# Optimization experiments

Measured on AMD Instinct MI355X. Metric: run time of the kernel, lower is better.

The kernel has to match this reference:

```python
import jax, jax.numpy as jnp
import numpy as np

B, T, C = 2, 2048, 2048
H, HD = 16, 128  # num_heads, head_dim; inner_dim = H*HD = C
EPS = 1e-8


def _hadamard(n):
    # Sylvester construction, orthonormal scaling 1/sqrt(n)
    h = np.array([[1.0]], dtype=np.float32)
    while h.shape[0] < n:
        h = np.block([[h, h], [h, -h]])
    return jnp.asarray(h / np.sqrt(n), dtype=jnp.float32)


def _round_ste(x):
    # straight-through rounding (matches int8 training-time quantization semantics)
    return x + jax.lax.stop_gradient(jnp.round(x) - x)


def q8_linear(x, w):
    # dynamic per-token int8 activation quant + per-out-channel int8 weight quant
    s_x = jnp.max(jnp.abs(x), axis=-1, keepdims=True) / 127.0 + EPS   # (B,T,1)
    xq = _round_ste(jnp.clip(x / s_x, -127.0, 127.0))
    s_w = jnp.max(jnp.abs(w), axis=-1, keepdims=True) / 127.0 + EPS   # (O,1)
    wq = _round_ste(jnp.clip(w / s_w, -127.0, 127.0))
    return jnp.einsum('btk,ok->bto', xq, wq) * s_x * s_w[:, 0]


def rmsnorm(x, g, eps=1e-6):
    return x * jax.lax.rsqrt(jnp.mean(x * x, axis=-1, keepdims=True) + eps) * g


def apply_rope(x, cos, sin):
    # x: (B,T,H*HD); cos/sin: (T,HD/2); interleaved rotary per head
    b, t, c = x.shape
    xh = x.reshape(b, t, -1, HD)
    x1, x2 = xh[..., 0::2], xh[..., 1::2]
    co = cos[None, :, None, :]
    si = sin[None, :, None, :]
    o1 = x1 * co - x2 * si
    o2 = x1 * si + x2 * co
    out = jnp.stack([o1, o2], axis=-1).reshape(b, t, -1, HD)
    return out.reshape(b, t, c)


def setup_inputs() -> dict:
    key = jax.random.key(0)
    ks = jax.random.split(key, 8)
    hidden_states = jax.random.normal(ks[0], (B, T, C), jnp.float32)
    attention_mask = jax.random.randint(ks[1], (B,), 1, T + 1).astype(jnp.int32)  # valid lengths
    sc = 1.0 / np.sqrt(C)
    wq = jax.random.normal(ks[2], (H * HD, C), jnp.float32) * sc
    wk = jax.random.normal(ks[3], (H * HD, C), jnp.float32) * sc
    wv = jax.random.normal(ks[4], (H * HD, C), jnp.float32) * sc
    wo = jax.random.normal(ks[5], (C, H * HD), jnp.float32) * (1.0 / np.sqrt(H * HD))
    q_gamma = jnp.ones((H * HD,), jnp.float32)
    k_gamma = jnp.ones((H * HD,), jnp.float32)
    inv_freq = 1.0 / (10000.0 ** (np.arange(0, HD, 2, dtype=np.float32) / HD))
    freqs = np.outer(np.arange(T, dtype=np.float32), inv_freq)  # (T, HD/2)
    cos = jnp.asarray(np.cos(freqs), jnp.float32)
    sin = jnp.asarray(np.sin(freqs), jnp.float32)
    return {"hidden_states": hidden_states, "attention_mask": attention_mask,
            "wq": wq, "wk": wk, "wv": wv, "wo": wo,
            "q_gamma": q_gamma, "k_gamma": k_gamma, "cos": cos, "sin": sin}


def reference(hidden_states, attention_mask, wq, wk, wv, wo, q_gamma, k_gamma, cos, sin):
    b, t, c = hidden_states.shape
    q = rmsnorm(q8_linear(hidden_states, wq), q_gamma)
    k = rmsnorm(q8_linear(hidden_states, wk), k_gamma)
    v = q8_linear(hidden_states, wv)
    q = apply_rope(q, cos, sin)
    k = apply_rope(k, cos, sin)
    # (B,T,H*HD) -> (B,H,T,HD)
    q = q.reshape(b, t, H, HD).transpose(0, 2, 1, 3)
    k = k.reshape(b, t, H, HD).transpose(0, 2, 1, 3)
    v = v.reshape(b, t, H, HD).transpose(0, 2, 1, 3)
    # Hadamard rotation of q/k head dims (orthonormal -> preserves qk dot products)
    Hm = _hadamard(HD)
    qh = q @ Hm
    kh = k @ Hm
    scores = jnp.einsum('bhqd,bhkd->bhqk', qh, kh) * (1.0 / np.sqrt(HD))
    # ragged batch mask: keys beyond per-batch valid length are masked out
    valid = jnp.arange(t)[None, :] < attention_mask[:, None]   # (B,T)
    scores = jnp.where(valid[:, None, None, :], scores, -1e9)
    p = jax.nn.softmax(scores, axis=-1)
    o = jnp.einsum('bhqk,bhkd->bhqd', p, v)
    o = o.transpose(0, 2, 1, 3).reshape(b, t, c)
    return q8_linear(o, wo)
```

## Files before the change

kernel.cpp:

```cpp
#include <hip/hip_runtime.h>
#include <stdint.h>

typedef unsigned short u16;
typedef unsigned int u32;
typedef int v4i __attribute__((ext_vector_type(4)));
typedef float v4f __attribute__((ext_vector_type(4)));
typedef short v8s __attribute__((ext_vector_type(8)));

#define Bn 2
#define Tn 2048
#define Cn 2048
#define Hn 16
#define HDn 128

__device__ __forceinline__ float b2f(u16 u) {
    u32 x = ((u32)u) << 16;
    float f;
    __builtin_memcpy(&f, &x, 4);
    return f;
}
__device__ __forceinline__ u16 f2b(float f) {
    u32 x;
    __builtin_memcpy(&x, &f, 4);
    u32 r = (x + 0x7fffu + ((x >> 16) & 1u)) >> 16;
    return (u16)r;
}

__device__ __forceinline__ void async16(const void* g, void* l) {
    __builtin_amdgcn_global_load_lds(
        (const __attribute__((address_space(1))) u32*)g,
        (__attribute__((address_space(3))) u32*)l, 16, 0, 0);
}

__global__ __launch_bounds__(256) void quant_all(
    const float* __restrict__ w0, const float* __restrict__ w1,
    const float* __restrict__ w2, const float* __restrict__ w3,
    const float* __restrict__ hid, int8_t* __restrict__ Q,
    float* __restrict__ S) {
    int r = blockIdx.x;
    const float* src;
    int ro;
    if (r < 2048) { src = w0; ro = r; }
    else if (r < 4096) { src = w1; ro = r - 2048; }
    else if (r < 6144) { src = w2; ro = r - 4096; }
    else if (r < 8192) { src = w3; ro = r - 6144; }
    else { src = hid; ro = r - 8192; }
    const float* x = src + (size_t)ro * Cn;
    int tid = threadIdx.x;
    float4 v0 = ((const float4*)x)[tid * 2];
    float4 v1 = ((const float4*)x)[tid * 2 + 1];
    float a[8] = {v0.x, v0.y, v0.z, v0.w, v1.x, v1.y, v1.z, v1.w};
    float m = 0.f;
#pragma unroll
    for (int i = 0; i < 8; i++) m = fmaxf(m, fabsf(a[i]));
#pragma unroll
    for (int o = 32; o; o >>= 1) m = fmaxf(m, __shfl_xor(m, o));
    __shared__ float sm[4];
    if ((tid & 63) == 0) sm[tid >> 6] = m;
    __syncthreads();
    m = fmaxf(fmaxf(sm[0], sm[1]), fmaxf(sm[2], sm[3]));
    float s = m * (1.0f / 127.0f) + 1e-8f;
    if (tid == 0) S[r] = s;
    u32 lo = 0, hi = 0;
#pragma unroll
    for (int i = 0; i < 8; i++) {
        float q = rintf(fminf(127.f, fmaxf(-127.f, a[i] / s)));
        int qi = (int)q;
        u32 byte = (u32)(qi & 0xff);
        if (i < 4) lo |= byte << (8 * i);
        else hi |= byte << (8 * (i - 4));
    }
    u32* qp = (u32*)(Q + (size_t)r * Cn);
    qp[tid * 2] = lo;
    qp[tid * 2 + 1] = hi;
}

__global__ __launch_bounds__(256) void quant_rows(const float* __restrict__ X,
                                                  int8_t* __restrict__ Q,
                                                  float* __restrict__ S) {
    int r = blockIdx.x;
    const float* x = X + (size_t)r * Cn;
    int tid = threadIdx.x;
    float4 v0 = ((const float4*)x)[tid * 2];
    float4 v1 = ((const float4*)x)[tid * 2 + 1];
    float a[8] = {v0.x, v0.y, v0.z, v0.w, v1.x, v1.y, v1.z, v1.w};
    float m = 0.f;
#pragma unroll
    for (int i = 0; i < 8; i++) m = fmaxf(m, fabsf(a[i]));
#pragma unroll
    for (int o = 32; o; o >>= 1) m = fmaxf(m, __shfl_xor(m, o));
    __shared__ float sm[4];
    if ((tid & 63) == 0) sm[tid >> 6] = m;
    __syncthreads();
    m = fmaxf(fmaxf(sm[0], sm[1]), fmaxf(sm[2], sm[3]));
    float s = m * (1.0f / 127.0f) + 1e-8f;
    if (tid == 0) S[r] = s;
    u32 lo = 0, hi = 0;
#pragma unroll
    for (int i = 0; i < 8; i++) {
        float q = rintf(fminf(127.f, fmaxf(-127.f, a[i] / s)));
        int qi = (int)q;
        u32 byte = (u32)(qi & 0xff);
        if (i < 4) lo |= byte << (8 * i);
        else hi |= byte << (8 * (i - 4));
    }
    u32* qp = (u32*)(Q + (size_t)r * Cn);
    qp[tid * 2] = lo;
    qp[tid * 2 + 1] = hi;
}

__global__ __launch_bounds__(256) void gemm_i8(
    const int8_t* __restrict__ A, const int8_t* __restrict__ Bw,
    const float* __restrict__ sA, const float* __restrict__ sB,
    void* __restrict__ Co, long long bStride, long long sbStride,
    long long cStride, int fp32out) {
    int z = blockIdx.z;
    Bw += (size_t)z * bStride;
    sB += (size_t)z * sbStride;
    const int K = 2048, N = 2048;
    __shared__ int8_t As[128 * 64];
    __shared__ int8_t Bs[128 * 64];
    int m0 = blockIdx.x * 128, n0 = blockIdx.y * 128;
    int tid = threadIdx.x, w = tid >> 6, lane = tid & 63;
    int quad = lane >> 4, l15 = lane & 15;
    int wy = w >> 1, wx = w & 1;
    const v4i zi = {0, 0, 0, 0};
    v4i acc[4][4];
#pragma unroll
    for (int i = 0; i < 4; i++)
#pragma unroll
        for (int j = 0; j < 4; j++) acc[i][j] = zi;
    int lrow = lane >> 2;
    int slot = lane & 3;
    int srow = w * 32 + lrow;
    int klog = ((slot ^ (lrow & 3)) * 16);
    const int8_t* ga = A + (size_t)(m0 + srow) * K + klog;
    const int8_t* gb = Bw + (size_t)(n0 + srow) * K + klog;
    int8_t* la = &As[srow * 64 + slot * 16];
    int8_t* lb = &Bs[srow * 64 + slot * 16];
    for (int k0 = 0; k0 < K; k0 += 64) {
        async16(ga + k0, la);
        async16(ga + k0 + (size_t)16 * K, la + 16 * 64);
        async16(gb + k0, lb);
        async16(gb + k0 + (size_t)16 * K, lb + 16 * 64);
        __syncthreads();
        int swz = (quad ^ (l15 & 3)) * 16;
        v4i af[4], bf4[4];
#pragma unroll
        for (int i = 0; i < 4; i++)
            af[i] = *(const v4i*)&As[(wy * 64 + i * 16 + l15) * 64 + swz];
#pragma unroll
        for (int j = 0; j < 4; j++)
            bf4[j] = *(const v4i*)&Bs[(wx * 64 + j * 16 + l15) * 64 + swz];
#pragma unroll
        for (int i = 0; i < 4; i++)
#pragma unroll
            for (int j = 0; j < 4; j++)
                acc[i][j] = __builtin_amdgcn_mfma_i32_16x16x64_i8(
                    af[i], bf4[j], acc[i][j], 0, 0, 0);
        __syncthreads();
    }
#pragma unroll
    for (int i = 0; i < 4; i++) {
        int mb = m0 + wy * 64 + i * 16 + quad * 4;
        float s0 = sA[mb], s1 = sA[mb + 1], s2 = sA[mb + 2], s3 = sA[mb + 3];
#pragma unroll
        for (int j = 0; j < 4; j++) {
            int n = n0 + wx * 64 + j * 16 + l15;
            float sb = sB[n];
            if (fp32out) {
                float* cp = (float*)Co + (size_t)cStride * z + (size_t)mb * N + n;
                cp[0] = (float)acc[i][j][0] * s0 * sb;
                cp[N] = (float)acc[i][j][1] * s1 * sb;
                cp[2 * N] = (float)acc[i][j][2] * s2 * sb;
                cp[3 * N] = (float)acc[i][j][3] * s3 * sb;
            } else {
                u16* cp = (u16*)Co + (size_t)cStride * z + (size_t)mb * N + n;
                cp[0] = f2b((float)acc[i][j][0] * s0 * sb);
                cp[N] = f2b((float)acc[i][j][1] * s1 * sb);
                cp[2 * N] = f2b((float)acc[i][j][2] * s2 * sb);
                cp[3 * N] = f2b((float)acc[i][j][3] * s3 * sb);
            }
        }
    }
}

__global__ __launch_bounds__(256) void norm_rope2(u16* __restrict__ Qb,
                                                  u16* __restrict__ Kb,
                                                  const float* __restrict__ qg,
                                                  const float* __restrict__ kg,
                                                  const float* __restrict__ cs,
                                                  const float* __restrict__ sn) {
    int row = blockIdx.x;
    int isq = row < 4096;
    row &= 4095;
    u16* x = (isq ? Qb : Kb) + (size_t)row * Cn;
    const float* g = isq ? qg : kg;
    float ps = isq ? 0.08838834764831845f : 1.0f;
    int t = row & (Tn - 1);
    int tid = threadIdx.x;
    uint4 raw = ((const uint4*)x)[tid];
    u16 us[8];
    us[0] = raw.x & 0xffff; us[1] = raw.x >> 16;
    us[2] = raw.y & 0xffff; us[3] = raw.y >> 16;
    us[4] = raw.z & 0xffff; us[5] = raw.z >> 16;
    us[6] = raw.w & 0xffff; us[7] = raw.w >> 16;
    float v[8];
#pragma unroll
    for (int i = 0; i < 8; i++) v[i] = b2f(us[i]);
    float ss = 0.f;
#pragma unroll
    for (int i = 0; i < 8; i++) ss += v[i] * v[i];
#pragma unroll
    for (int o = 32; o; o >>= 1) ss += __shfl_xor(ss, o);
    __shared__ float sm[4];
    if ((tid & 63) == 0) sm[tid >> 6] = ss;
    __syncthreads();
    ss = sm[0] + sm[1] + sm[2] + sm[3];
    float r = rsqrtf(ss * (1.f / 2048.f) + 1e-6f) * ps;
    float4 g0 = ((const float4*)g)[tid * 2];
    float4 g1 = ((const float4*)g)[tid * 2 + 1];
    float n[8];
    n[0] = v[0] * r * g0.x; n[1] = v[1] * r * g0.y;
    n[2] = v[2] * r * g0.z; n[3] = v[3] * r * g0.w;
    n[4] = v[4] * r * g1.x; n[5] = v[5] * r * g1.y;
    n[6] = v[6] * r * g1.z; n[7] = v[7] * r * g1.w;
    int pi = (tid & 15) * 4;
    float4 c4 = *(const float4*)(cs + t * 64 + pi);
    float4 s4 = *(const float4*)(sn + t * 64 + pi);
    float o[8];
    o[0] = n[0] * c4.x - n[1] * s4.x; o[1] = n[0] * s4.x + n[1] * c4.x;
    o[2] = n[2] * c4.y - n[3] * s4.y; o[3] = n[2] * s4.y + n[3] * c4.y;
    o[4] = n[4] * c4.z - n[5] * s4.z; o[5] = n[4] * s4.z + n[5] * c4.z;
    o[6] = n[6] * c4.w - n[7] * s4.w; o[7] = n[6] * s4.w + n[7] * c4.w;
    uint4 out;
    out.x = (u32)f2b(o[0]) | ((u32)f2b(o[1]) << 16);
    out.y = (u32)f2b(o[2]) | ((u32)f2b(o[3]) << 16);
    out.z = (u32)f2b(o[4]) | ((u32)f2b(o[5]) << 16);
    out.w = (u32)f2b(o[6]) | ((u32)f2b(o[7]) << 16);
    ((uint4*)x)[tid] = out;
}

__global__ __launch_bounds__(256) void vtrans(const u16* __restrict__ V,
                                              u16* __restrict__ Vt) {
    int bh = blockIdx.y;
    int b = bh >> 4, h = bh & 15;
    int t0 = blockIdx.x * 64;
    __shared__ u32 tile[64][133];
    int tid = threadIdx.x;
    int r = tid >> 2, seg = (tid & 3) * 32;
    const uint4* src =
        (const uint4*)(V + ((size_t)b * Tn + t0 + r) * Cn + h * HDn + seg);
#pragma unroll
    for (int i = 0; i < 4; i++) {
        uint4 u = src[i];
        u32 uu[4] = {u.x, u.y, u.z, u.w};
#pragma unroll
        for (int j = 0; j < 4; j++) {
            tile[r][seg + i * 8 + j * 2] = uu[j] & 0xffff;
            tile[r][seg + i * 8 + j * 2 + 1] = uu[j] >> 16;
        }
    }
    __syncthreads();
    int d = tid >> 1, tseg = (tid & 1) * 32;
    u16* dst = Vt + ((size_t)bh * HDn + d) * Tn + t0 + tseg;
#pragma unroll
    for (int i = 0; i < 4; i++) {
        u32 p0 = tile[tseg + i * 8 + 0][d] | (tile[tseg + i * 8 + 1][d] << 16);
        u32 p1 = tile[tseg + i * 8 + 2][d] | (tile[tseg + i * 8 + 3][d] << 16);
        u32 p2 = tile[tseg + i * 8 + 4][d] | (tile[tseg + i * 8 + 5][d] << 16);
        u32 p3 = tile[tseg + i * 8 + 6][d] | (tile[tseg + i * 8 + 7][d] << 16);
        ((uint4*)dst)[i] = make_uint4(p0, p1, p2, p3);
    }
}

__global__ __launch_bounds__(256, 3) void flash(const u16* __restrict__ Qb,
                                                const u16* __restrict__ Kb,
                                                const u16* __restrict__ Vt,
                                                const int* __restrict__ mask,
                                                float* __restrict__ O) {
    int qt = blockIdx.x, bh = blockIdx.y;
    int b = bh >> 4, h = bh & 15;
    int L = mask[b];
    int nkfull = L >> 6;
    int nk = (L + 63) >> 6;
    __shared__ u16 Ks[64 * 128];
    __shared__ u16 Vs[128 * 64];
    __shared__ u16 Ps[64 * 72];
    __shared__ float sred[256];
    __shared__ float sinv[64];
    int tid = threadIdx.x, w = tid >> 6, lane = tid & 63;
    int quad = lane >> 4, l15 = lane & 15;

    v8s aq[4][4];
#pragma unroll
    for (int i = 0; i < 4; i++)
#pragma unroll
        for (int kk = 0; kk < 4; kk++)
            aq[i][kk] = *(const v8s*)(Qb +
                                      ((size_t)b * Tn + qt * 64 + i * 16 + l15) * Cn +
                                      h * HDn + kk * 32 + quad * 8);

    const u16* ksp[4];
    u16* kdp[4];
    const u16* vsp[4];
    u16* vdp[4];
#pragma unroll
    for (int cc = 0; cc < 4; cc++) {
        int c = w * 4 + cc;
        int rk = c * 4 + (lane >> 4);
        int sk = lane & 15;
        int lgk = sk ^ (rk & 7);
        ksp[cc] = Kb + ((size_t)b * Tn + rk) * Cn + h * HDn + lgk * 8;
        kdp[cc] = Ks + rk * 128 + sk * 8;
        int rv = c * 8 + (lane >> 3);
        int sv = lane & 7;
        int lgv = sv ^ (rv & 7);
        vsp[cc] = Vt + ((size_t)bh * HDn + rv) * Tn + lgv * 8;
        vdp[cc] = Vs + rv * 64 + sv * 8;
    }

    float sum16[16];
#pragma unroll
    for (int j = 0; j < 16; j++) sum16[j] = 0.f;
    const v4f zf = {0.f, 0.f, 0.f, 0.f};
    v4f oacc[4][2];
#pragma unroll
    for (int m = 0; m < 4; m++) {
        oacc[m][0] = zf;
        oacc[m][1] = zf;
    }
    int swz = ((l15 & 7) ^ quad) << 3;

    for (int kt = 0; kt < nk; kt++) {
        __syncthreads();
#pragma unroll
        for (int cc = 0; cc < 4; cc++) async16(ksp[cc], kdp[cc]);
#pragma unroll
        for (int cc = 0; cc < 4; cc++) async16(vsp[cc], vdp[cc]);
#pragma unroll
        for (int cc = 0; cc < 4; cc++) {
            ksp[cc] += 64 * Cn;
            vsp[cc] += 64;
        }
        __syncthreads();
        v4f sacc[4] = {zf, zf, zf, zf};
        const u16* krow = Ks + (w * 16 + l15) * 128;
#pragma unroll
        for (int kk = 0; kk < 4; kk++) {
            v8s bk = *(const v8s*)(krow + ((((kk * 4 + quad) ^ (l15 & 7))) << 3));
#pragma unroll
            for (int i = 0; i < 4; i++)
                sacc[i] = __builtin_amdgcn_mfma_f32_16x16x32_bf16(aq[i][kk], bk,
                                                                  sacc[i], 0, 0, 0);
        }
        bool valid = (kt < nkfull) || ((kt * 64 + w * 16 + l15) < L);
#pragma unroll
        for (int i = 0; i < 4; i++)
#pragma unroll
            for (int r2 = 0; r2 < 4; r2++) {
                float p = valid ? __expf(sacc[i][r2]) : 0.f;
                sum16[i * 4 + r2] += p;
                Ps[(i * 16 + quad * 4 + r2) * 72 + w * 16 + l15] = f2b(p);
            }
        __syncthreads();
#pragma unroll
        for (int kk2 = 0; kk2 < 2; kk2++) {
            v8s ap[4];
#pragma unroll
            for (int m = 0; m < 4; m++)
                ap[m] = *(const v8s*)(Ps + (m * 16 + l15) * 72 + kk2 * 32 + quad * 8);
#pragma unroll
            for (int nbi = 0; nbi < 2; nbi++) {
                int vr = (2 * w + nbi) * 16 + l15;
                v8s bv = *(const v8s*)(Vs + vr * 64 +
                                       ((((kk2 * 4 + quad) ^ (l15 & 7))) << 3));
#pragma unroll
                for (int m = 0; m < 4; m++)
                    oacc[m][nbi] = __builtin_amdgcn_mfma_f32_16x16x32_bf16(
                        ap[m], bv, oacc[m][nbi], 0, 0, 0);
            }
        }
    }
#pragma unroll
    for (int j = 0; j < 16; j++) {
        float s = sum16[j];
        s += __shfl_xor(s, 1);
        s += __shfl_xor(s, 2);
        s += __shfl_xor(s, 4);
        s += __shfl_xor(s, 8);
        sum16[j] = s;
    }
    if (l15 == 0) {
#pragma unroll
        for (int i = 0; i < 4; i++)
#pragma unroll
            for (int r2 = 0; r2 < 4; r2++)
                sred[w * 64 + i * 16 + quad * 4 + r2] = sum16[i * 4 + r2];
    }
    __syncthreads();
    if (tid < 64)
        sinv[tid] =
            1.f / (sred[tid] + sred[64 + tid] + sred[128 + tid] + sred[192 + tid]);
    __syncthreads();
#pragma unroll
    for (int m = 0; m < 4; m++)
#pragma unroll
        for (int r2 = 0; r2 < 4; r2++) {
            float inv = sinv[m * 16 + quad * 4 + r2];
            int row = qt * 64 + m * 16 + quad * 4 + r2;
#pragma unroll
            for (int nbi = 0; nbi < 2; nbi++) {
                int d = h * HDn + (2 * w + nbi) * 16 + l15;
                O[((size_t)b * Tn + row) * Cn + d] = oacc[m][nbi][r2] * inv;
            }
        }
    (void)swz;
}

extern "C" void kernel_launch(void* const* d_in, const int* in_sizes, int n_in,
                              void* d_out, int out_size, void* d_ws,
                              size_t ws_size, hipStream_t stream) {
    const float* hidden = (const float*)d_in[0];
    const int* mask = (const int*)d_in[1];
    const float* wq = (const float*)d_in[2];
    const float* wk = (const float*)d_in[3];
    const float* wv = (const float*)d_in[4];
    const float* wo = (const float*)d_in[5];
    const float* qg = (const float*)d_in[6];
    const float* kg = (const float*)d_in[7];
    const float* cs = (const float*)d_in[8];
    const float* sn = (const float*)d_in[9];

    char* ws = (char*)d_ws;
    int8_t* q8 = (int8_t*)(ws);
    float* sAll = (float*)(ws + 25165824);
    u16* qb = (u16*)(ws + 25214976);
    u16* kb = (u16*)(ws + 41992192);
    u16* vb = (u16*)(ws + 58769408);
    u16* vt = (u16*)(ws + 75546624);
    float* Obuf = (float*)(ws + 92323840);
    int8_t* hid8 = q8 + 16777216;
    float* sx = sAll + 8192;

    quant_all<<<12288, 256, 0, stream>>>(wq, wk, wv, wo, hidden, q8, sAll);

    gemm_i8<<<dim3(32, 16, 3), 256, 0, stream>>>(hid8, q8, sx, sAll, (void*)qb,
                                                 4194304LL, 2048LL, 8388608LL, 0);

    norm_rope2<<<8192, 256, 0, stream>>>(qb, kb, qg, kg, cs, sn);
    vtrans<<<dim3(32, 32), 256, 0, stream>>>(vb, vt);

    flash<<<dim3(32, 32), 256, 0, stream>>>(qb, kb, vt, mask, Obuf);

    quant_rows<<<4096, 256, 0, stream>>>(Obuf, hid8, sx);
    gemm_i8<<<dim3(32, 16, 1), 256, 0, stream>>>(hid8, q8 + 12582912, sx,
                                                 sAll + 6144, d_out, 0LL, 0LL,
                                                 0LL, 1);
}
```

Measured before the change: 357.1 us.

## Double-buffer K/V tiles in flash attention to prefetch the next block

The flash attention kernel now keeps two LDS buffers each for K and V. The first tile is loaded before the loop, and each iteration issues async loads for the next tile before computing on the current one, which drops one barrier per iteration. The aim is to hide global-to-LDS latency behind the QK MFMA work. The price is twice the K/V shared memory, and the launch-bounds occupancy hint falls from 3 to 2 blocks. The mid-iteration barrier probably still waits on the outstanding prefetch, which limits how much overlap is possible.

```diff
diff --git a/kernel.cpp b/kernel.cpp
--- a/kernel.cpp
+++ b/kernel.cpp
@@ -274,7 +274,7 @@
     }
 }
 
-__global__ __launch_bounds__(256, 3) void flash(const u16* __restrict__ Qb,
+__global__ __launch_bounds__(256, 2) void flash(const u16* __restrict__ Qb,
                                                 const u16* __restrict__ Kb,
                                                 const u16* __restrict__ Vt,
                                                 const int* __restrict__ mask,
@@ -284,8 +284,8 @@
     int L = mask[b];
     int nkfull = L >> 6;
     int nk = (L + 63) >> 6;
-    __shared__ u16 Ks[64 * 128];
-    __shared__ u16 Vs[128 * 64];
+    __shared__ u16 Ks[2][64 * 128];
+    __shared__ u16 Vs[2][128 * 64];
     __shared__ u16 Ps[64 * 72];
     __shared__ float sred[256];
     __shared__ float sinv[64];
@@ -302,9 +302,8 @@
                                       h * HDn + kk * 32 + quad * 8);
 
     const u16* ksp[4];
-    u16* kdp[4];
     const u16* vsp[4];
-    u16* vdp[4];
+    int kdo[4], vdo[4];
 #pragma unroll
     for (int cc = 0; cc < 4; cc++) {
         int c = w * 4 + cc;
@@ -312,12 +311,12 @@
         int sk = lane & 15;
         int lgk = sk ^ (rk & 7);
         ksp[cc] = Kb + ((size_t)b * Tn + rk) * Cn + h * HDn + lgk * 8;
-        kdp[cc] = Ks + rk * 128 + sk * 8;
+        kdo[cc] = rk * 128 + sk * 8;
         int rv = c * 8 + (lane >> 3);
         int sv = lane & 7;
         int lgv = sv ^ (rv & 7);
         vsp[cc] = Vt + ((size_t)bh * HDn + rv) * Tn + lgv * 8;
-        vdp[cc] = Vs + rv * 64 + sv * 8;
+        vdo[cc] = rv * 64 + sv * 8;
     }
 
     float sum16[16];
@@ -330,22 +329,29 @@
         oacc[m][0] = zf;
         oacc[m][1] = zf;
     }
-    int swz = ((l15 & 7) ^ quad) << 3;
-
+
+#pragma unroll
+    for (int cc = 0; cc < 4; cc++) {
+        async16(ksp[cc], &Ks[0][kdo[cc]]);
+        async16(vsp[cc], &Vs[0][vdo[cc]]);
+        ksp[cc] += (size_t)64 * Cn;
+        vsp[cc] += 64;
+    }
+
+    int cur = 0;
     for (int kt = 0; kt < nk; kt++) {
         __syncthreads();
-#pragma unroll
-        for (int cc = 0; cc < 4; cc++) async16(ksp[cc], kdp[cc]);
-#pragma unroll
-        for (int cc = 0; cc < 4; cc++) async16(vsp[cc], vdp[cc]);
-#pragma unroll
-        for (int cc = 0; cc < 4; cc++) {
-            ksp[cc] += 64 * Cn;
-            vsp[cc] += 64;
-        }
-        __syncthreads();
+        if (kt + 1 < nk) {
+#pragma unroll
+            for (int cc = 0; cc < 4; cc++) {
+                async16(ksp[cc], &Ks[cur ^ 1][kdo[cc]]);
+                async16(vsp[cc], &Vs[cur ^ 1][vdo[cc]]);
+                ksp[cc] += (size_t)64 * Cn;
+                vsp[cc] += 64;
+            }
+        }
         v4f sacc[4] = {zf, zf, zf, zf};
-        const u16* krow = Ks + (w * 16 + l15) * 128;
+        const u16* krow = &Ks[cur][(w * 16 + l15) * 128];
 #pragma unroll
         for (int kk = 0; kk < 4; kk++) {
             v8s bk = *(const v8s*)(krow + ((((kk * 4 + quad) ^ (l15 & 7))) << 3));
@@ -373,14 +379,15 @@
 #pragma unroll
             for (int nbi = 0; nbi < 2; nbi++) {
                 int vr = (2 * w + nbi) * 16 + l15;
-                v8s bv = *(const v8s*)(Vs + vr * 64 +
-                                       ((((kk2 * 4 + quad) ^ (l15 & 7))) << 3));
+                v8s bv = *(const v8s*)(&Vs[cur][vr * 64 +
+                                       ((((kk2 * 4 + quad) ^ (l15 & 7))) << 3)]);
 #pragma unroll
                 for (int m = 0; m < 4; m++)
                     oacc[m][nbi] = __builtin_amdgcn_mfma_f32_16x16x32_bf16(
                         ap[m], bv, oacc[m][nbi], 0, 0, 0);
             }
         }
+        cur ^= 1;
     }
 #pragma unroll
     for (int j = 0; j < 16; j++) {
@@ -415,7 +422,6 @@
                 O[((size_t)b * Tn + row) * Cn + d] = oacc[m][nbi][r2] * inv;
             }
         }
-    (void)swz;
 }
 
 extern "C" void kernel_launch(void* const* d_in, const int* in_sizes, int n_in,
```

Result: faster. 343.5 us (-3.8%).
